# Performance work log

Measured on AMD Instinct MI355X. Metric: run time of the kernel, lower is better.

Reference implementation:

```python
import jax, jax.numpy as jnp
import numpy as np

B, T, D, M, H = 1, 256, 512, 64, 8
HD = D // H              # head_dim = 64
IN = 2 * HD + 2 * M      # crossing_net input dim = 256
HID = D // 2             # crossing_net hidden = 256


def setup_inputs() -> dict:
    key = jax.random.key(0)
    ks = jax.random.split(key, 14)
    s = 0.02
    return {
        "x": jax.random.normal(ks[0], (B, T, D), jnp.float32),
        "coords": jax.random.normal(ks[1], (B, T, M), jnp.float32),
        "Wq": jax.random.normal(ks[2], (D, D), jnp.float32) * s,
        "Wk": jax.random.normal(ks[3], (D, D), jnp.float32) * s,
        "Wv": jax.random.normal(ks[4], (D, D), jnp.float32) * s,
        "Wo": jax.random.normal(ks[5], (D, D), jnp.float32) * s,
        "W1": jax.random.normal(ks[6], (IN, HID), jnp.float32) * s,
        "b1": jnp.zeros((HID,), jnp.float32),
        "W2": jax.random.normal(ks[7], (HID, 2), jnp.float32) * s,
        "b2": jnp.zeros((2,), jnp.float32),
        "W3": jax.random.normal(ks[8], (D, D), jnp.float32) * s,
        "b3": jnp.zeros((D,), jnp.float32),
        "W4": jax.random.normal(ks[9], (D, D), jnp.float32) * s,
        "b4": jnp.zeros((D,), jnp.float32),
    }


def reference(x, coords, Wq, Wk, Wv, Wo, W1, b1, W2, b2, W3, b3, W4, b4):
    b, t, d = x.shape
    m = coords.shape[-1]
    hd = d // H
    # projections -> (B, H, T, HD)
    q = (x @ Wq).reshape(b, t, H, hd).transpose(0, 2, 1, 3)
    k = (x @ Wk).reshape(b, t, H, hd).transpose(0, 2, 1, 3)
    v = (x @ Wv).reshape(b, t, H, hd).transpose(0, 2, 1, 3)
    # crossing_net layer1 on concat([q_i, k_j, c_i, c_j]) decomposes by blocks of W1:
    W1q, W1k = W1[:hd], W1[hd:2 * hd]
    W1ci, W1cj = W1[2 * hd:2 * hd + m], W1[2 * hd + m:]
    a_i = jnp.einsum('bhid,df->bhif', q, W1q) + jnp.einsum('bim,mf->bif', coords, W1ci)[:, None]
    a_j = jnp.einsum('bhjd,df->bhjf', k, W1k) + jnp.einsum('bjm,mf->bjf', coords, W1cj)[:, None] + b1
    # (B,H,T,T,HID) pairwise hidden, then layer2 -> 2 logits
    h = jax.nn.silu(a_i[:, :, :, None, :] + a_j[:, :, None, :, :])
    z = jnp.einsum('bhijf,fc->bhijc', h, W2) + b2
    crossings = jax.nn.softmax(z, axis=-1)            # (B,H,T,T,2)
    linking = crossings[..., 0] - crossings[..., 1]   # (B,H,T,T)
    scores = linking / np.float32(np.sqrt(hd))
    causal = jnp.triu(jnp.ones((t, t), bool), 1)
    scores = jnp.where(causal, -jnp.inf, scores)
    attn = jax.nn.softmax(scores, axis=-1)
    out = jnp.einsum('bhij,bhjd->bhid', attn, v)
    out = out.transpose(0, 2, 1, 3).reshape(b, t, d)
    out = jax.nn.silu(out @ W3 + b3) @ W4 + b4        # invariant_net
    out = out @ Wo                                    # to_out
    writhe = linking.sum(axis=(-1, -2))               # (B,H)
    linking_mean = jnp.abs(linking).mean()
    return out, writhe, linking_mean
```

## Files before the change

### kernel.cpp

```cpp
#include <hip/hip_runtime.h>
#include <math.h>

#define T_ 256
#define D_ 512
#define M_ 64
#define H_ 8
#define HD_ 64
#define HID_ 256


#define SILU_ACC(acc, w, aa, bb, ea, eb) \
    { float u_ = (aa) + (bb); \
      float e_ = (ea) * (eb); \
      float sg_ = __builtin_amdgcn_rcpf(1.f + e_); \
      acc = fmaf((w) * u_, sg_, acc); }

#define GEMM_INNER \
    _Pragma("unroll") \
    for (int kk = 0; kk < 32; ++kk) { \
        float a0 = As[ty * 2 + 0][kk]; \
        float a1 = As[ty * 2 + 1][kk]; \
        float b0 = Bs[kk][tx * 2 + 0]; \
        float b1 = Bs[kk][tx * 2 + 1]; \
        a00 = fmaf(a0, b0, a00); a01 = fmaf(a0, b1, a01); \
        a10 = fmaf(a1, b0, a10); a11 = fmaf(a1, b1, a11); }

__global__ __launch_bounds__(256) void k1_kernel(
    const float* __restrict__ x,
    const float* __restrict__ Wq, const float* __restrict__ Wk,
    const float* __restrict__ Wv, const float* __restrict__ W4,
    const float* __restrict__ Wo, const float* __restrict__ b4,
    float* __restrict__ y, float* __restrict__ W4o, float* __restrict__ b4o)
{
    __shared__ __align__(16) float As[32][36];
    __shared__ __align__(16) float Bs[32][36];

    const int job = blockIdx.x;
    const int tid = threadIdx.x;
    const int tx = tid & 15, ty = tid >> 4;
    const int r4 = tid >> 3, c4 = tid & 7;

    if (job < 640) {
        const float* A;
        const float* B;
        float* C;
        int row0, col0;
        if (job < 384) {
            const int z = job >> 7, rem = job & 127;
            row0 = (rem >> 4) << 5; col0 = (rem & 15) << 5;
            A = x;
            B = (z == 0) ? Wq : (z == 1) ? Wk : Wv;
            C = y + (long)z * (T_ * D_);
        } else {
            const int idx = job - 384;
            row0 = (idx >> 4) << 5; col0 = (idx & 15) << 5;
            A = W4; B = Wo; C = W4o;
        }
        float a00 = 0.f, a01 = 0.f, a10 = 0.f, a11 = 0.f;
        for (int k0 = 0; k0 < D_; k0 += 32) {
            *(float4*)&As[r4][c4 * 4] = *(const float4*)(A + (long)(row0 + r4) * D_ + k0 + c4 * 4);
            *(float4*)&Bs[r4][c4 * 4] = *(const float4*)(B + (long)(k0 + r4) * D_ + col0 + c4 * 4);
            __syncthreads();
            GEMM_INNER
            __syncthreads();
        }
        C[(long)(row0 + ty * 2 + 0) * D_ + col0 + tx * 2 + 0] = a00;
        C[(long)(row0 + ty * 2 + 0) * D_ + col0 + tx * 2 + 1] = a01;
        C[(long)(row0 + ty * 2 + 1) * D_ + col0 + tx * 2 + 0] = a10;
        C[(long)(row0 + ty * 2 + 1) * D_ + col0 + tx * 2 + 1] = a11;
    } else {
        const int c = (job - 640) * 256 + tid;
        float s = 0.f;
        for (int k = 0; k < D_; k += 4) {
            s = fmaf(b4[k + 0], Wo[(long)(k + 0) * D_ + c], s);
            s = fmaf(b4[k + 1], Wo[(long)(k + 1) * D_ + c], s);
            s = fmaf(b4[k + 2], Wo[(long)(k + 2) * D_ + c], s);
            s = fmaf(b4[k + 3], Wo[(long)(k + 3) * D_ + c], s);
        }
        b4o[c] = s;
    }
}

__global__ __launch_bounds__(256) void aiaj_kernel(
    const float* __restrict__ y, const float* __restrict__ coords,
    const float* __restrict__ W1, const float* __restrict__ b1,
    float* __restrict__ abuf, float* __restrict__ ebuf)
{
    __shared__ __align__(16) float As[32][36];
    __shared__ __align__(16) float Bs[32][36];
    const int z = blockIdx.z;
    const int sel = z >> 3, h = z & 7;
    const float* Ay = y + (long)sel * (T_ * D_) + h * HD_;
    float* C = abuf + (long)z * (T_ * HID_);
    float* E = ebuf + (long)z * (T_ * HID_);
    const int tid = threadIdx.x;
    const int tx = tid & 15, ty = tid >> 4;
    const int row0 = blockIdx.y * 32, col0 = blockIdx.x * 32;
    const int r4 = tid >> 3, c4 = tid & 7;
    float a00 = 0.f, a01 = 0.f, a10 = 0.f, a11 = 0.f;
    for (int k0 = 0; k0 < 128; k0 += 32) {
        if (k0 < 64) {
            *(float4*)&As[r4][c4 * 4] =
                *(const float4*)(Ay + (long)(row0 + r4) * D_ + k0 + c4 * 4);
            *(float4*)&Bs[r4][c4 * 4] =
                *(const float4*)(W1 + (long)(sel * 64 + k0 + r4) * HID_ + col0 + c4 * 4);
        } else {
            *(float4*)&As[r4][c4 * 4] =
                *(const float4*)(coords + (long)(row0 + r4) * M_ + (k0 - 64) + c4 * 4);
            *(float4*)&Bs[r4][c4 * 4] =
                *(const float4*)(W1 + (long)(128 + 64 * sel + k0 - 64 + r4) * HID_ + col0 + c4 * 4);
        }
        __syncthreads();
        GEMM_INNER
        __syncthreads();
    }
    const int c0 = col0 + tx * 2, r0 = row0 + ty * 2;
    float bb0 = (sel == 1) ? b1[c0 + 0] : 0.f;
    float bb1 = (sel == 1) ? b1[c0 + 1] : 0.f;
    float v00 = a00 + bb0, v01 = a01 + bb1;
    float v10 = a10 + bb0, v11 = a11 + bb1;
    C[(long)(r0 + 0) * HID_ + c0 + 0] = v00;
    C[(long)(r0 + 0) * HID_ + c0 + 1] = v01;
    C[(long)(r0 + 1) * HID_ + c0 + 0] = v10;
    C[(long)(r0 + 1) * HID_ + c0 + 1] = v11;
    E[(long)(r0 + 0) * HID_ + c0 + 0] = __expf(-v00);
    E[(long)(r0 + 0) * HID_ + c0 + 1] = __expf(-v01);
    E[(long)(r0 + 1) * HID_ + c0 + 0] = __expf(-v10);
    E[(long)(r0 + 1) * HID_ + c0 + 1] = __expf(-v11);
}

__global__ __launch_bounds__(256) void pairwise_kernel(
    const float* __restrict__ a_i, const float* __restrict__ a_j,
    const float* __restrict__ e_i, const float* __restrict__ e_j,
    const float* __restrict__ W2, float* __restrict__ pb)
{
    const int jt = blockIdx.x;
    const int it = blockIdx.y;
    const int hs = blockIdx.z;
    const int h = hs >> 1, fb = (hs & 1) * 128;
    const int t = threadIdx.x;

    __shared__ __align__(16) float ai_s[32][132];
    __shared__ __align__(16) float aj_s[32][132];
    __shared__ __align__(16) float ei_s[32][132];
    __shared__ __align__(16) float ej_s[32][132];
    __shared__ __align__(16) float w2d[128];

    if (t < 128) w2d[t] = W2[(fb + t) * 2 + 0] - W2[(fb + t) * 2 + 1];

    const long iof = ((long)h * T_ + it * 32) * HID_ + fb;
    const long jof = ((long)h * T_ + jt * 32) * HID_ + fb;
    #pragma unroll
    for (int l = 0; l < 4; ++l) {
        int idx = t + l * 256;
        int r = idx >> 5, c4 = idx & 31;
        long ro = (long)r * HID_ + c4 * 4;
        *(float4*)&ai_s[r][c4 * 4] = *(const float4*)(a_i + iof + ro);
        *(float4*)&aj_s[r][c4 * 4] = *(const float4*)(a_j + jof + ro);
        *(float4*)&ei_s[r][c4 * 4] = *(const float4*)(e_i + iof + ro);
        *(float4*)&ej_s[r][c4 * 4] = *(const float4*)(e_j + jof + ro);
    }
    __syncthreads();

    const int ty = t >> 4, tx = t & 15;
    float s00 = 0.f, s01 = 0.f, s10 = 0.f, s11 = 0.f;

    #pragma unroll 4
    for (int f4 = 0; f4 < 32; ++f4) {
        float4 a0 = *(const float4*)&ai_s[ty][f4 * 4];
        float4 a1 = *(const float4*)&ai_s[ty + 16][f4 * 4];
        float4 c0 = *(const float4*)&aj_s[tx][f4 * 4];
        float4 c1 = *(const float4*)&aj_s[tx + 16][f4 * 4];
        float4 p0 = *(const float4*)&ei_s[ty][f4 * 4];
        float4 p1 = *(const float4*)&ei_s[ty + 16][f4 * 4];
        float4 q0 = *(const float4*)&ej_s[tx][f4 * 4];
        float4 q1 = *(const float4*)&ej_s[tx + 16][f4 * 4];
        float4 w  = *(const float4*)&w2d[f4 * 4];
        SILU_ACC(s00, w.x, a0.x, c0.x, p0.x, q0.x); SILU_ACC(s01, w.x, a0.x, c1.x, p0.x, q1.x);
        SILU_ACC(s10, w.x, a1.x, c0.x, p1.x, q0.x); SILU_ACC(s11, w.x, a1.x, c1.x, p1.x, q1.x);
        SILU_ACC(s00, w.y, a0.y, c0.y, p0.y, q0.y); SILU_ACC(s01, w.y, a0.y, c1.y, p0.y, q1.y);
        SILU_ACC(s10, w.y, a1.y, c0.y, p1.y, q0.y); SILU_ACC(s11, w.y, a1.y, c1.y, p1.y, q1.y);
        SILU_ACC(s00, w.z, a0.z, c0.z, p0.z, q0.z); SILU_ACC(s01, w.z, a0.z, c1.z, p0.z, q1.z);
        SILU_ACC(s10, w.z, a1.z, c0.z, p1.z, q0.z); SILU_ACC(s11, w.z, a1.z, c1.z, p1.z, q1.z);
        SILU_ACC(s00, w.w, a0.w, c0.w, p0.w, q0.w); SILU_ACC(s01, w.w, a0.w, c1.w, p0.w, q1.w);
        SILU_ACC(s10, w.w, a1.w, c0.w, p1.w, q0.w); SILU_ACC(s11, w.w, a1.w, c1.w, p1.w, q1.w);
    }

    const int gi0 = it * 32 + ty, gi1 = gi0 + 16;
    const int gj0 = jt * 32 + tx, gj1 = gj0 + 16;
    float* pbh = pb + (long)hs * (T_ * T_);
    pbh[(long)gi0 * T_ + gj0] = s00;
    pbh[(long)gi0 * T_ + gj1] = s01;
    pbh[(long)gi1 * T_ + gj0] = s10;
    pbh[(long)gi1 * T_ + gj1] = s11;
}

__global__ __launch_bounds__(512) void attn_kernel(
    const float* __restrict__ pb, const float* __restrict__ yv,
    const float* __restrict__ b2, float* __restrict__ o,
    float* __restrict__ parts)
{
    const int i = blockIdx.x, t = threadIdx.x;
    const int w = t >> 6, lane = t & 63;
    __shared__ float p[8][256];
    __shared__ float psc[8];
    const float b2d = b2[0] - b2[1];
    const float* pb0 = pb + ((long)(2 * w + 0) * T_ + i) * T_;
    const float* pb1 = pb + ((long)(2 * w + 1) * T_ + i) * T_;
    float sv[4];
    float mx = -1e30f, wsum = 0.f, asum = 0.f;
    #pragma unroll
    for (int r = 0; r < 4; ++r) {
        int j = lane + r * 64;
        float s = (pb0[j] + pb1[j]) + b2d;
        float as = fabsf(s);
        float e = __expf(-as);
        float tv = (1.f - e) * __builtin_amdgcn_rcpf(1.f + e);
        float lk = (s < 0.f) ? -tv : tv;
        wsum += lk; asum += fabsf(lk);
        float sc = (j <= i) ? lk * 0.125f : -1e30f;
        sv[r] = sc; mx = fmaxf(mx, sc);
    }
    #pragma unroll
    for (int off = 32; off > 0; off >>= 1) mx = fmaxf(mx, __shfl_xor(mx, off));
    float sum = 0.f;
    #pragma unroll
    for (int r = 0; r < 4; ++r) {
        int j = lane + r * 64;
        float e = (j <= i) ? __expf(sv[r] - mx) : 0.f;
        p[w][j] = e; sum += e;
    }
    #pragma unroll
    for (int off = 32; off > 0; off >>= 1) {
        sum  += __shfl_xor(sum, off);
        wsum += __shfl_xor(wsum, off);
        asum += __shfl_xor(asum, off);
    }
    if (lane == 0) {
        psc[w] = __builtin_amdgcn_rcpf(sum);
        parts[((long)i * 8 + w) * 2 + 0] = wsum;
        parts[((long)i * 8 + w) * 2 + 1] = asum;
    }
    __syncthreads();
    const float pinv = psc[w];
    const float* vb = yv + t;
    float a0 = 0.f, a1 = 0.f, a2 = 0.f, a3 = 0.f;
    float a4 = 0.f, a5 = 0.f, a6 = 0.f, a7 = 0.f;
    int j = 0;
    for (; j + 7 <= i; j += 8) {
        a0 = fmaf(p[w][j + 0], vb[(long)(j + 0) * D_], a0);
        a1 = fmaf(p[w][j + 1], vb[(long)(j + 1) * D_], a1);
        a2 = fmaf(p[w][j + 2], vb[(long)(j + 2) * D_], a2);
        a3 = fmaf(p[w][j + 3], vb[(long)(j + 3) * D_], a3);
        a4 = fmaf(p[w][j + 4], vb[(long)(j + 4) * D_], a4);
        a5 = fmaf(p[w][j + 5], vb[(long)(j + 5) * D_], a5);
        a6 = fmaf(p[w][j + 6], vb[(long)(j + 6) * D_], a6);
        a7 = fmaf(p[w][j + 7], vb[(long)(j + 7) * D_], a7);
    }
    for (; j <= i; ++j) a0 = fmaf(p[w][j], vb[(long)j * D_], a0);
    o[(long)i * D_ + t] = (((a0 + a1) + (a2 + a3)) + ((a4 + a5) + (a6 + a7))) * pinv;
}

__global__ __launch_bounds__(256) void epA_kernel(
    const float* __restrict__ o, const float* __restrict__ W3,
    float* __restrict__ hbuf)
{
    __shared__ __align__(16) float As[32][36];
    __shared__ __align__(16) float Bs[32][36];
    const int z = blockIdx.z;
    float* C = hbuf + (long)z * (T_ * D_);
    const int tid = threadIdx.x;
    const int tx = tid & 15, ty = tid >> 4;
    const int row0 = blockIdx.y * 32, col0 = blockIdx.x * 32;
    const int r4 = tid >> 3, c4 = tid & 7;
    float a00 = 0.f, a01 = 0.f, a10 = 0.f, a11 = 0.f;
    for (int k0 = z * 128; k0 < z * 128 + 128; k0 += 32) {
        *(float4*)&As[r4][c4 * 4] = *(const float4*)(o + (long)(row0 + r4) * D_ + k0 + c4 * 4);
        *(float4*)&Bs[r4][c4 * 4] = *(const float4*)(W3 + (long)(k0 + r4) * D_ + col0 + c4 * 4);
        __syncthreads();
        GEMM_INNER
        __syncthreads();
    }
    C[(long)(row0 + ty * 2 + 0) * D_ + col0 + tx * 2 + 0] = a00;
    C[(long)(row0 + ty * 2 + 0) * D_ + col0 + tx * 2 + 1] = a01;
    C[(long)(row0 + ty * 2 + 1) * D_ + col0 + tx * 2 + 0] = a10;
    C[(long)(row0 + ty * 2 + 1) * D_ + col0 + tx * 2 + 1] = a11;
}

__global__ __launch_bounds__(256) void epF_kernel(
    const float* __restrict__ hbuf, const float* __restrict__ b3,
    const float* __restrict__ W4o, const float* __restrict__ b4o,
    float* __restrict__ out, const float* __restrict__ parts,
    float* __restrict__ tailo)
{
    __shared__ __align__(16) float As[32][36];
    __shared__ __align__(16) float Bs[32][36];
    const int tid = threadIdx.x;
    const int tx = tid & 15, ty = tid >> 4;
    const int row0 = blockIdx.y * 32, col0 = blockIdx.x * 32;
    const int r4 = tid >> 3, c4 = tid & 7;
    float a00 = 0.f, a01 = 0.f, a10 = 0.f, a11 = 0.f;
    for (int k0 = 0; k0 < D_; k0 += 32) {
        {
            long off = (long)(row0 + r4) * D_ + k0 + c4 * 4;
            float4 v0 = *(const float4*)(hbuf + off);
            float4 v1 = *(const float4*)(hbuf + 131072 + off);
            float4 v2 = *(const float4*)(hbuf + 262144 + off);
            float4 v3 = *(const float4*)(hbuf + 393216 + off);
            float4 bb = *(const float4*)(b3 + k0 + c4 * 4);
            float4 g;
            g.x = ((v0.x + v1.x) + (v2.x + v3.x)) + bb.x;
            g.y = ((v0.y + v1.y) + (v2.y + v3.y)) + bb.y;
            g.z = ((v0.z + v1.z) + (v2.z + v3.z)) + bb.z;
            g.w = ((v0.w + v1.w) + (v2.w + v3.w)) + bb.w;
            g.x = g.x * __builtin_amdgcn_rcpf(1.f + __expf(-g.x));
            g.y = g.y * __builtin_amdgcn_rcpf(1.f + __expf(-g.y));
            g.z = g.z * __builtin_amdgcn_rcpf(1.f + __expf(-g.z));
            g.w = g.w * __builtin_amdgcn_rcpf(1.f + __expf(-g.w));
            *(float4*)&As[r4][c4 * 4] = g;
        }
        *(float4*)&Bs[r4][c4 * 4] = *(const float4*)(W4o + (long)(k0 + r4) * D_ + col0 + c4 * 4);
        __syncthreads();
        GEMM_INNER
        __syncthreads();
    }
    const int c0 = col0 + tx * 2;
    out[(long)(row0 + ty * 2 + 0) * D_ + c0 + 0] = a00 + b4o[c0 + 0];
    out[(long)(row0 + ty * 2 + 0) * D_ + c0 + 1] = a01 + b4o[c0 + 1];
    out[(long)(row0 + ty * 2 + 1) * D_ + c0 + 0] = a10 + b4o[c0 + 0];
    out[(long)(row0 + ty * 2 + 1) * D_ + c0 + 1] = a11 + b4o[c0 + 1];

    if (blockIdx.x == 0 && blockIdx.y == 0 && tid < 64) {
        const int lane = tid;
        if (lane < 8) {
            float wsum = 0.f;
            for (int i = 0; i < 256; ++i) wsum += parts[((long)i * 8 + lane) * 2 + 0];
            tailo[lane] = wsum;
        }
        float a = 0.f;
        for (int idx = lane; idx < 2048; idx += 64) a += parts[(long)idx * 2 + 1];
        #pragma unroll
        for (int off = 32; off > 0; off >>= 1) a += __shfl_xor(a, off);
        if (lane == 0) tailo[8] = a / (float)(H_ * T_ * T_);
    }
}

extern "C" void kernel_launch(void* const* d_in, const int* in_sizes, int n_in,
                              void* d_out, int out_size, void* d_ws, size_t ws_size,
                              hipStream_t stream)
{
    const float* x      = (const float*)d_in[0];
    const float* coords = (const float*)d_in[1];
    const float* Wq     = (const float*)d_in[2];
    const float* Wk     = (const float*)d_in[3];
    const float* Wv     = (const float*)d_in[4];
    const float* Wo     = (const float*)d_in[5];
    const float* W1     = (const float*)d_in[6];
    const float* b1     = (const float*)d_in[7];
    const float* W2     = (const float*)d_in[8];
    const float* b2     = (const float*)d_in[9];
    const float* W3     = (const float*)d_in[10];
    const float* b3     = (const float*)d_in[11];
    const float* W4     = (const float*)d_in[12];
    const float* b4     = (const float*)d_in[13];
    float* out = (float*)d_out;

    float* ws = (float*)d_ws;
    float* y     = ws;
    float* ai    = ws + 393216;
    float* aj    = ws + 917504;
    float* ei    = ws + 1441792;
    float* ej    = ws + 1966080;
    float* pb    = ws + 2490368;
    float* o     = ws + 3538944;
    float* parts = ws + 3670016;
    float* W4o   = ws + 3674112;
    float* b4o   = ws + 3936256;
    float* hb    = pb;

    k1_kernel<<<dim3(642), dim3(256), 0, stream>>>(x, Wq, Wk, Wv, W4, Wo, b4,
                                                   y, W4o, b4o);

    aiaj_kernel<<<dim3(8, 8, 16), dim3(256), 0, stream>>>(y, coords, W1, b1, ai, ei);

    pairwise_kernel<<<dim3(8, 8, 16), dim3(256), 0, stream>>>(ai, aj, ei, ej, W2, pb);

    attn_kernel<<<dim3(T_), dim3(512), 0, stream>>>(pb, y + 2 * (T_ * D_), b2, o, parts);

    epA_kernel<<<dim3(16, 8, 4), dim3(256), 0, stream>>>(o, W3, hb);

    epF_kernel<<<dim3(16, 8), dim3(256), 0, stream>>>(hb, b3, W4o, b4o, out,
                                                      parts, out + 131072);
}
```

Before: 110.1 us.

## Enlarge pairwise i-tile to 64 rows and stage features in two phases

The pairwise kernel now computes a 64x32 (i,j) tile per block instead of 32x32, with 8 accumulators per thread, and loads the 128-feature slice in two 64-wide phases to keep shared memory small. This increases reuse of the j-side operands loaded into registers and halves the number of blocks and redundant j-tile loads. In exchange it launches only 512 blocks, which reduces parallelism and adds a barrier between phases.

```diff
diff --git a/kernel.cpp b/kernel.cpp
--- a/kernel.cpp
+++ b/kernel.cpp
@@ -140,59 +140,93 @@
     const int h = hs >> 1, fb = (hs & 1) * 128;
     const int t = threadIdx.x;
 
-    __shared__ __align__(16) float ai_s[32][132];
-    __shared__ __align__(16) float aj_s[32][132];
-    __shared__ __align__(16) float ei_s[32][132];
-    __shared__ __align__(16) float ej_s[32][132];
+    __shared__ __align__(16) float ai_s[64][68];
+    __shared__ __align__(16) float ei_s[64][68];
+    __shared__ __align__(16) float aj_s[32][68];
+    __shared__ __align__(16) float ej_s[32][68];
     __shared__ __align__(16) float w2d[128];
 
     if (t < 128) w2d[t] = W2[(fb + t) * 2 + 0] - W2[(fb + t) * 2 + 1];
 
-    const long iof = ((long)h * T_ + it * 32) * HID_ + fb;
-    const long jof = ((long)h * T_ + jt * 32) * HID_ + fb;
+    const int ty = t >> 4, tx = t & 15;
+    float acc00 = 0.f, acc01 = 0.f, acc10 = 0.f, acc11 = 0.f;
+    float acc20 = 0.f, acc21 = 0.f, acc30 = 0.f, acc31 = 0.f;
+
     #pragma unroll
-    for (int l = 0; l < 4; ++l) {
-        int idx = t + l * 256;
-        int r = idx >> 5, c4 = idx & 31;
-        long ro = (long)r * HID_ + c4 * 4;
-        *(float4*)&ai_s[r][c4 * 4] = *(const float4*)(a_i + iof + ro);
-        *(float4*)&aj_s[r][c4 * 4] = *(const float4*)(a_j + jof + ro);
-        *(float4*)&ei_s[r][c4 * 4] = *(const float4*)(e_i + iof + ro);
-        *(float4*)&ej_s[r][c4 * 4] = *(const float4*)(e_j + jof + ro);
-    }
-    __syncthreads();
-
-    const int ty = t >> 4, tx = t & 15;
-    float s00 = 0.f, s01 = 0.f, s10 = 0.f, s11 = 0.f;
-
-    #pragma unroll 4
-    for (int f4 = 0; f4 < 32; ++f4) {
-        float4 a0 = *(const float4*)&ai_s[ty][f4 * 4];
-        float4 a1 = *(const float4*)&ai_s[ty + 16][f4 * 4];
-        float4 c0 = *(const float4*)&aj_s[tx][f4 * 4];
-        float4 c1 = *(const float4*)&aj_s[tx + 16][f4 * 4];
-        float4 p0 = *(const float4*)&ei_s[ty][f4 * 4];
-        float4 p1 = *(const float4*)&ei_s[ty + 16][f4 * 4];
-        float4 q0 = *(const float4*)&ej_s[tx][f4 * 4];
-        float4 q1 = *(const float4*)&ej_s[tx + 16][f4 * 4];
-        float4 w  = *(const float4*)&w2d[f4 * 4];
-        SILU_ACC(s00, w.x, a0.x, c0.x, p0.x, q0.x); SILU_ACC(s01, w.x, a0.x, c1.x, p0.x, q1.x);
-        SILU_ACC(s10, w.x, a1.x, c0.x, p1.x, q0.x); SILU_ACC(s11, w.x, a1.x, c1.x, p1.x, q1.x);
-        SILU_ACC(s00, w.y, a0.y, c0.y, p0.y, q0.y); SILU_ACC(s01, w.y, a0.y, c1.y, p0.y, q1.y);
-        SILU_ACC(s10, w.y, a1.y, c0.y, p1.y, q0.y); SILU_ACC(s11, w.y, a1.y, c1.y, p1.y, q1.y);
-        SILU_ACC(s00, w.z, a0.z, c0.z, p0.z, q0.z); SILU_ACC(s01, w.z, a0.z, c1.z, p0.z, q1.z);
-        SILU_ACC(s10, w.z, a1.z, c0.z, p1.z, q0.z); SILU_ACC(s11, w.z, a1.z, c1.z, p1.z, q1.z);
-        SILU_ACC(s00, w.w, a0.w, c0.w, p0.w, q0.w); SILU_ACC(s01, w.w, a0.w, c1.w, p0.w, q1.w);
-        SILU_ACC(s10, w.w, a1.w, c0.w, p1.w, q0.w); SILU_ACC(s11, w.w, a1.w, c1.w, p1.w, q1.w);
-    }
-
-    const int gi0 = it * 32 + ty, gi1 = gi0 + 16;
+    for (int ph = 0; ph < 2; ++ph) {
+        if (ph) __syncthreads();
+        const long iof = ((long)h * T_ + it * 64) * HID_ + fb + ph * 64;
+        const long jof = ((long)h * T_ + jt * 32) * HID_ + fb + ph * 64;
+        #pragma unroll
+        for (int l = 0; l < 4; ++l) {
+            int idx = t + l * 256;
+            int r = idx >> 4, c4 = idx & 15;
+            long ro = (long)r * HID_ + c4 * 4;
+            *(float4*)&ai_s[r][c4 * 4] = *(const float4*)(a_i + iof + ro);
+            *(float4*)&ei_s[r][c4 * 4] = *(const float4*)(e_i + iof + ro);
+        }
+        #pragma unroll
+        for (int l = 0; l < 2; ++l) {
+            int idx = t + l * 256;
+            int r = idx >> 4, c4 = idx & 15;
+            long ro = (long)r * HID_ + c4 * 4;
+            *(float4*)&aj_s[r][c4 * 4] = *(const float4*)(a_j + jof + ro);
+            *(float4*)&ej_s[r][c4 * 4] = *(const float4*)(e_j + jof + ro);
+        }
+        __syncthreads();
+
+        const float* wp = &w2d[ph * 64];
+        #pragma unroll 2
+        for (int f4 = 0; f4 < 16; ++f4) {
+            float4 w  = *(const float4*)&wp[f4 * 4];
+            float4 c0 = *(const float4*)&aj_s[tx][f4 * 4];
+            float4 c1 = *(const float4*)&aj_s[tx + 16][f4 * 4];
+            float4 q0 = *(const float4*)&ej_s[tx][f4 * 4];
+            float4 q1 = *(const float4*)&ej_s[tx + 16][f4 * 4];
+
+            float4 a, p;
+            a = *(const float4*)&ai_s[ty][f4 * 4];
+            p = *(const float4*)&ei_s[ty][f4 * 4];
+            SILU_ACC(acc00, w.x, a.x, c0.x, p.x, q0.x); SILU_ACC(acc01, w.x, a.x, c1.x, p.x, q1.x);
+            SILU_ACC(acc00, w.y, a.y, c0.y, p.y, q0.y); SILU_ACC(acc01, w.y, a.y, c1.y, p.y, q1.y);
+            SILU_ACC(acc00, w.z, a.z, c0.z, p.z, q0.z); SILU_ACC(acc01, w.z, a.z, c1.z, p.z, q1.z);
+            SILU_ACC(acc00, w.w, a.w, c0.w, p.w, q0.w); SILU_ACC(acc01, w.w, a.w, c1.w, p.w, q1.w);
+
+            a = *(const float4*)&ai_s[ty + 16][f4 * 4];
+            p = *(const float4*)&ei_s[ty + 16][f4 * 4];
+            SILU_ACC(acc10, w.x, a.x, c0.x, p.x, q0.x); SILU_ACC(acc11, w.x, a.x, c1.x, p.x, q1.x);
+            SILU_ACC(acc10, w.y, a.y, c0.y, p.y, q0.y); SILU_ACC(acc11, w.y, a.y, c1.y, p.y, q1.y);
+            SILU_ACC(acc10, w.z, a.z, c0.z, p.z, q0.z); SILU_ACC(acc11, w.z, a.z, c1.z, p.z, q1.z);
+            SILU_ACC(acc10, w.w, a.w, c0.w, p.w, q0.w); SILU_ACC(acc11, w.w, a.w, c1.w, p.w, q1.w);
+
+            a = *(const float4*)&ai_s[ty + 32][f4 * 4];
+            p = *(const float4*)&ei_s[ty + 32][f4 * 4];
+            SILU_ACC(acc20, w.x, a.x, c0.x, p.x, q0.x); SILU_ACC(acc21, w.x, a.x, c1.x, p.x, q1.x);
+            SILU_ACC(acc20, w.y, a.y, c0.y, p.y, q0.y); SILU_ACC(acc21, w.y, a.y, c1.y, p.y, q1.y);
+            SILU_ACC(acc20, w.z, a.z, c0.z, p.z, q0.z); SILU_ACC(acc21, w.z, a.z, c1.z, p.z, q1.z);
+            SILU_ACC(acc20, w.w, a.w, c0.w, p.w, q0.w); SILU_ACC(acc21, w.w, a.w, c1.w, p.w, q1.w);
+
+            a = *(const float4*)&ai_s[ty + 48][f4 * 4];
+            p = *(const float4*)&ei_s[ty + 48][f4 * 4];
+            SILU_ACC(acc30, w.x, a.x, c0.x, p.x, q0.x); SILU_ACC(acc31, w.x, a.x, c1.x, p.x, q1.x);
+            SILU_ACC(acc30, w.y, a.y, c0.y, p.y, q0.y); SILU_ACC(acc31, w.y, a.y, c1.y, p.y, q1.y);
+            SILU_ACC(acc30, w.z, a.z, c0.z, p.z, q0.z); SILU_ACC(acc31, w.z, a.z, c1.z, p.z, q1.z);
+            SILU_ACC(acc30, w.w, a.w, c0.w, p.w, q0.w); SILU_ACC(acc31, w.w, a.w, c1.w, p.w, q1.w);
+        }
+    }
+
+    float* pbh = pb + (long)hs * (T_ * T_);
     const int gj0 = jt * 32 + tx, gj1 = gj0 + 16;
-    float* pbh = pb + (long)hs * (T_ * T_);
-    pbh[(long)gi0 * T_ + gj0] = s00;
-    pbh[(long)gi0 * T_ + gj1] = s01;
-    pbh[(long)gi1 * T_ + gj0] = s10;
-    pbh[(long)gi1 * T_ + gj1] = s11;
+    {
+        int gi = it * 64 + ty;
+        pbh[(long)gi * T_ + gj0] = acc00;  pbh[(long)gi * T_ + gj1] = acc01;
+        gi += 16;
+        pbh[(long)gi * T_ + gj0] = acc10;  pbh[(long)gi * T_ + gj1] = acc11;
+        gi += 16;
+        pbh[(long)gi * T_ + gj0] = acc20;  pbh[(long)gi * T_ + gj1] = acc21;
+        gi += 16;
+        pbh[(long)gi * T_ + gj0] = acc30;  pbh[(long)gi * T_ + gj1] = acc31;
+    }
 }
 
 __global__ __launch_bounds__(512) void attn_kernel(
@@ -383,7 +417,7 @@
 
     aiaj_kernel<<<dim3(8, 8, 16), dim3(256), 0, stream>>>(y, coords, W1, b1, ai, ei);
 
-    pairwise_kernel<<<dim3(8, 8, 16), dim3(256), 0, stream>>>(ai, aj, ei, ej, W2, pb);
+    pairwise_kernel<<<dim3(8, 4, 16), dim3(256), 0, stream>>>(ai, aj, ei, ej, W2, pb);
 
     attn_kernel<<<dim3(T_), dim3(512), 0, stream>>>(pb, y + 2 * (T_ * D_), b2, o, parts);
 
```

Measured after the change: 111.8 us. About the same (+1.5%).
